# Optimization experiments

Measured on AMD Instinct MI355X. Metric: run time of the kernel, lower is better.

## Reference

```python
import jax, jax.numpy as jnp
import numpy as np

P, G, UV = 5, 40000, 256          # n_parts, gs_num (visible UV texels), uv_size
ZD, FD, HD = 32, 64, 32           # latent_z_dim, latent_f_dim, latent_h_dim
H1, L1 = 128, 3                   # mlp1 hidden dim, fc layers
H2, L2 = 128, 3                   # mlp2 hidden dim, fc layers
CC, LC = 64, 4                    # cnn hidden channels, cnn hidden layers


def _mlp_params(key, din, hid, nlayers, dout, nparts):
    ks = jax.random.split(key, 3)
    s = lambda f: 1.0 / np.sqrt(f)
    return dict(
        w_in=jax.random.normal(ks[0], (nparts, din, hid), jnp.float32) * s(din),
        b_in=jnp.zeros((nparts, hid), jnp.float32),
        w_hid=jax.random.normal(ks[1], (nparts, nlayers - 1, hid, hid), jnp.float32) * s(hid),
        b_hid=jnp.zeros((nparts, nlayers - 1, hid), jnp.float32),
        w_out=jax.random.normal(ks[2], (nparts, hid, dout), jnp.float32) * s(hid),
        b_out=jnp.zeros((nparts, dout), jnp.float32),
    )


def setup_inputs() -> dict:
    key = jax.random.key(0)
    ks = jax.random.split(key, 12)
    d1 = FD + ZD
    d2 = d1 + 3 + 11
    inp = {
        'latent_z': jax.random.normal(ks[2], (G, ZD), jnp.float32),
        'latent_f': jax.random.normal(ks[3], (P, FD), jnp.float32),
        'cano_xyz': jax.random.normal(ks[4], (G, 3), jnp.float32),
    }
    for k, v in _mlp_params(ks[0], d1, H1, L1, 11, P).items():
        inp['mlp1_' + k] = v
    for k, v in _mlp_params(ks[1], d2, H2, L2, HD, P).items():
        inp['mlp2_' + k] = v
    inp['conv_in_w'] = jax.random.normal(ks[5], (CC, HD, 3, 3), jnp.float32) * (1.0 / np.sqrt(HD * 9))
    inp['conv_in_b'] = jnp.zeros((CC,), jnp.float32)
    inp['conv_hid_w'] = jax.random.normal(ks[6], (LC - 1, CC, CC, 3, 3), jnp.float32) * (1.0 / np.sqrt(CC * 9))
    inp['conv_hid_b'] = jnp.zeros((LC - 1, CC), jnp.float32)
    inp['conv_out_w'] = jax.random.normal(ks[7], (3, CC, 3, 3), jnp.float32) * (1.0 / np.sqrt(CC * 9))
    inp['conv_out_b'] = jnp.zeros((3,), jnp.float32)
    inp['gs_part'] = jax.random.randint(ks[8], (G,), 0, P, jnp.int32)
    inp['uv_idx'] = jax.random.permutation(ks[9], UV * UV)[:G].astype(jnp.int32)  # unique visible texels
    return inp


def _part_mlp(x, w_in, b_in, w_hid, b_hid, w_out, b_out, part):
    # x: [G, D]; weights stacked over parts. Run every part's MLP, gather by part id.
    h = jax.nn.leaky_relu(jnp.einsum('gd,pdh->pgh', x, w_in) + b_in[:, None, :])
    for l in range(w_hid.shape[1]):
        h = jax.nn.leaky_relu(jnp.einsum('pgh,pho->pgo', h, w_hid[:, l]) + b_hid[:, l][:, None, :])
    out = jnp.einsum('pgh,pho->pgo', h, w_out) + b_out[:, None, :]  # [P, G, O]
    return out[part, jnp.arange(out.shape[1])]                       # [G, O]


def _conv(x, w, b):
    y = jax.lax.conv_general_dilated(x, w, (1, 1), 'SAME',
                                     dimension_numbers=('NCHW', 'OIHW', 'NCHW'))
    return y + b[None, :, None, None]


def _instance_norm(x, eps=1e-5):
    m = x.mean(axis=(2, 3), keepdims=True)
    v = x.var(axis=(2, 3), keepdims=True)
    return (x - m) / jnp.sqrt(v + eps)


def reference(latent_z, latent_f, cano_xyz,
              mlp1_w_in, mlp1_b_in, mlp1_w_hid, mlp1_b_hid, mlp1_w_out, mlp1_b_out,
              mlp2_w_in, mlp2_b_in, mlp2_w_hid, mlp2_b_hid, mlp2_w_out, mlp2_b_out,
              conv_in_w, conv_in_b, conv_hid_w, conv_hid_b, conv_out_w, conv_out_b,
              gs_part, uv_idx):
    feat_f = latent_f[gs_part]                                  # [G, FD] per-part feature gather
    x1 = jnp.concatenate([feat_f, latent_z], axis=-1)           # [G, FD+ZD]
    attrs = _part_mlp(x1, mlp1_w_in, mlp1_b_in, mlp1_w_hid, mlp1_b_hid,
                      mlp1_w_out, mlp1_b_out, gs_part)          # [G, 11] gaussian attrs
    x2 = jnp.concatenate([x1, cano_xyz, attrs], axis=-1)        # [G, FD+ZD+3+11]
    h = _part_mlp(x2, mlp2_w_in, mlp2_b_in, mlp2_w_hid, mlp2_b_hid,
                  mlp2_w_out, mlp2_b_out, gs_part)              # [G, HD]
    # scatter per-gaussian features back into the UV map (uvmask-indexed texels)
    uvmap = jnp.zeros((UV * UV, h.shape[-1]), h.dtype).at[uv_idx].add(h)
    x = uvmap.T.reshape(1, h.shape[-1], UV, UV)                 # [1, HD, UV, UV]
    # CNN refinement: conv -> (relu, conv, instance_norm) x (LC-1) -> conv -> sigmoid
    x = _conv(x, conv_in_w, conv_in_b)
    for l in range(conv_hid_w.shape[0]):
        x = _instance_norm(_conv(jax.nn.relu(x), conv_hid_w[l], conv_hid_b[l]))
    x = _conv(x, conv_out_w, conv_out_b)
    return jax.nn.sigmoid(x)                                    # [1, 3, UV, UV]
```

## Files before the change

### kernel.cpp

```cpp
#include <hip/hip_runtime.h>

#define G_N 40000
#define P_N 5
#define PIX 65536
#define XP 136
#define CIP 72

typedef short short8 __attribute__((ext_vector_type(8)));
typedef short short4v __attribute__((ext_vector_type(4)));
typedef float f32x4 __attribute__((ext_vector_type(4)));
#define MFMA16(a, b, c) __builtin_amdgcn_mfma_f32_16x16x32_bf16(a, b, c, 0, 0, 0)

__device__ __forceinline__ short f2b(float f) {
    unsigned u = __builtin_bit_cast(unsigned, f);
    unsigned r = (u + 0x7fffu + ((u >> 16) & 1u)) >> 16;
    return (short)r;
}
__device__ __forceinline__ float b2f(short s) {
    unsigned u = ((unsigned)(unsigned short)s) << 16;
    return __builtin_bit_cast(float, u);
}


__global__ __launch_bounds__(256) void hist_k(const int* __restrict__ part,
                                              int* __restrict__ counts, int n) {
    __shared__ int s_c[P_N];
    if (threadIdx.x < P_N) s_c[threadIdx.x] = 0;
    __syncthreads();
    int g = blockIdx.x * 256 + threadIdx.x;
    if (g < n) atomicAdd(&s_c[part[g]], 1);
    __syncthreads();
    if (threadIdx.x < P_N) atomicAdd(&counts[threadIdx.x], s_c[threadIdx.x]);
}

__global__ void offs_k(const int* __restrict__ counts, int* __restrict__ offs) {
    if (threadIdx.x == 0) {
        int o = 0;
        for (int p = 0; p < P_N; ++p) {
            offs[p] = o;
            o += (counts[p] + 127) & ~127;
        }
        offs[P_N] = o;
    }
}

__global__ __launch_bounds__(256) void scatter_k(const int* __restrict__ part,
                                                 const int* __restrict__ offs,
                                                 int* __restrict__ cursors,
                                                 int* __restrict__ perm, int n) {
    const int t = threadIdx.x;
    const int g = blockIdx.x * 256 + t;
    const int p = (g < n) ? part[g] : -1;
    const int lane = t & 63;
    const int wid = t >> 6;
    __shared__ int s_wc[4][P_N];
    __shared__ int s_base[P_N];
    const unsigned long long lmask = (1ull << lane) - 1ull;
    int myrank = 0;
    for (int pp = 0; pp < P_N; ++pp) {
        unsigned long long m = __ballot(p == pp);
        if (p == pp) myrank = __popcll(m & lmask);
        if (lane == 0) s_wc[wid][pp] = __popcll(m);
    }
    __syncthreads();
    if (t < P_N) {
        int tot = s_wc[0][t] + s_wc[1][t] + s_wc[2][t] + s_wc[3][t];
        s_base[t] = atomicAdd(&cursors[t], tot);
    }
    __syncthreads();
    if (g < n) {
        int pre = 0;
        #pragma unroll
        for (int w2 = 0; w2 < 4; ++w2) if (w2 < wid) pre += s_wc[w2][p];
        perm[offs[p] + s_base[p] + pre + myrank] = g;
    }
}


__device__ __forceinline__ float mseg(int l, const float* __restrict__ src,
                                      int DIN, int DOUT, int NP, int pps) {
    const int pn = NP * 128;
    const int p = l / pn;
    const int r = l - p * pn;
    const int n = r >> 7, k = r & 127;
    return (n < DOUT && k < DIN) ? src[p * pps + k * DOUT + n] : 0.f;
}
__device__ __forceinline__ float cseg(int l, const float* __restrict__ src, int CIN) {
    const int per = 9 * 64 * CIN;
    const int ll = l / per;
    int rem = l - ll * per;
    const int tap = rem / (64 * CIN);
    rem -= tap * 64 * CIN;
    const int och = rem / CIN;
    const int ci = rem - och * CIN;
    return src[((ll * 64 + och) * CIN + ci) * 9 + tap];
}

__global__ __launch_bounds__(256) void prep_k(
        const float* __restrict__ m1wi, const float* __restrict__ m1wh,
        const float* __restrict__ m1wo, const float* __restrict__ m2wi,
        const float* __restrict__ m2wh, const float* __restrict__ m2wo,
        const float* __restrict__ cinw, const float* __restrict__ chw,
        short* __restrict__ wb) {
    const int idx = blockIdx.x * 256 + threadIdx.x;
    if (idx >= 651264) return;
    float v;
    if      (idx < 81920)  v = mseg(idx,          m1wi,         96, 128, 128, 12288);
    else if (idx < 163840) v = mseg(idx - 81920,  m1wh,        128, 128, 128, 32768);
    else if (idx < 245760) v = mseg(idx - 163840, m1wh + 16384,128, 128, 128, 32768);
    else if (idx < 256000) v = mseg(idx - 245760, m1wo,        128,  11,  16, 1408);
    else if (idx < 337920) v = mseg(idx - 256000, m2wi,        110, 128, 128, 14080);
    else if (idx < 419840) v = mseg(idx - 337920, m2wh,        128, 128, 128, 32768);
    else if (idx < 501760) v = mseg(idx - 419840, m2wh + 16384,128, 128, 128, 32768);
    else if (idx < 522240) v = mseg(idx - 501760, m2wo,        128,  32,  32, 4096);
    else if (idx < 540672) v = cseg(idx - 522240, cinw, 32);
    else                   v = cseg(idx - 540672, chw, 64);
    wb[idx] = f2b(v);
}


template<int NKC, bool ACT>
__device__ __forceinline__ void dlayerSep(const short* __restrict__ wt,
                                          const float* __restrict__ bias,
                                          const short* src, short* dst, int m0, int n0) {
    const int lane = threadIdx.x & 63;
    const int ln = lane & 15, lq = lane >> 4;
    short8 B[4][NKC];
    float bs[4];
    #pragma unroll
    for (int nt = 0; nt < 4; ++nt) {
        #pragma unroll
        for (int kc = 0; kc < NKC; ++kc)
            B[nt][kc] = *(const short8*)(wt + (n0 + nt * 16 + ln) * 128 + kc * 32 + lq * 8);
        bs[nt] = bias[n0 + nt * 16 + ln];
    }
    #pragma unroll
    for (int mt = 0; mt < 4; ++mt) {
        short8 A[NKC];
        #pragma unroll
        for (int kc = 0; kc < NKC; ++kc)
            A[kc] = *(const short8*)(src + (m0 + mt * 16 + ln) * XP + kc * 32 + lq * 8);
        #pragma unroll
        for (int nt = 0; nt < 4; ++nt) {
            f32x4 acc = {bs[nt], bs[nt], bs[nt], bs[nt]};
            #pragma unroll
            for (int kc = 0; kc < NKC; ++kc)
                acc = MFMA16(A[kc], B[nt][kc], acc);
            #pragma unroll
            for (int r = 0; r < 4; ++r) {
                float v = acc[r];
                if (ACT) v = fmaxf(v, 0.01f * v);
                dst[(m0 + mt * 16 + lq * 4 + r) * XP + n0 + nt * 16 + ln] = f2b(v);
            }
        }
    }
}

template<bool ACT>
__device__ __forceinline__ void dlayerIP(const short* __restrict__ wt,
                                         const float* __restrict__ bias,
                                         short* buf, int m0, int n0) {
    const int lane = threadIdx.x & 63;
    const int ln = lane & 15, lq = lane >> 4;
    short8 A[4][4];
    #pragma unroll
    for (int mt = 0; mt < 4; ++mt)
        #pragma unroll
        for (int kc = 0; kc < 4; ++kc)
            A[mt][kc] = *(const short8*)(buf + (m0 + mt * 16 + ln) * XP + kc * 32 + lq * 8);
    __syncthreads();
    #pragma unroll
    for (int nt = 0; nt < 4; ++nt) {
        short8 B[4];
        #pragma unroll
        for (int kc = 0; kc < 4; ++kc)
            B[kc] = *(const short8*)(wt + (n0 + nt * 16 + ln) * 128 + kc * 32 + lq * 8);
        const float bs = bias[n0 + nt * 16 + ln];
        #pragma unroll
        for (int mt = 0; mt < 4; ++mt) {
            f32x4 acc = {bs, bs, bs, bs};
            #pragma unroll
            for (int kc = 0; kc < 4; ++kc)
                acc = MFMA16(A[mt][kc], B[kc], acc);
            #pragma unroll
            for (int r = 0; r < 4; ++r) {
                float v = acc[r];
                if (ACT) v = fmaxf(v, 0.01f * v);
                buf[(m0 + mt * 16 + lq * 4 + r) * XP + n0 + nt * 16 + ln] = f2b(v);
            }
        }
    }
    __syncthreads();
}

__global__ __launch_bounds__(256) void mlp_k(
        const float* __restrict__ latent_z, const float* __restrict__ latent_f,
        const float* __restrict__ cano,
        const short* __restrict__ wt1i, const float* __restrict__ b1i,
        const short* __restrict__ wt1h0, const short* __restrict__ wt1h1,
        const float* __restrict__ b1h,
        const short* __restrict__ wt1o, const float* __restrict__ b1o,
        const short* __restrict__ wt2i, const float* __restrict__ b2i,
        const short* __restrict__ wt2h0, const short* __restrict__ wt2h1,
        const float* __restrict__ b2h,
        const short* __restrict__ wt2o, const float* __restrict__ b2o,
        const int* __restrict__ uv_idx, const int* __restrict__ perm,
        const int* __restrict__ offs, const int* __restrict__ counts,
        unsigned short* __restrict__ uvmap ) {
    __shared__ short s_x[128 * XP];
    __shared__ short s_h[128 * XP];
    __shared__ int s_g[128];
    __shared__ int s_uv[128];

    const int t = threadIdx.x;
    const int lane = t & 63;
    const int w = t >> 6;
    const int ln = lane & 15, lq = lane >> 4;
    const int pos0 = blockIdx.x * 128;
    if (pos0 >= offs[P_N]) return;
    int p = 0;
    #pragma unroll
    for (int q = 1; q < P_N; ++q) if (pos0 >= offs[q]) p = q;
    const int vend = offs[p] + counts[p];

    if (t < 128) {
        const int pos = pos0 + t;
        const int g = (pos < vend) ? perm[pos] : -1;
        s_g[t] = g;
        s_uv[t] = (g >= 0) ? uv_idx[g] : 0;
    }
    __syncthreads();

    for (int i = t; i < 128 * 16; i += 256) {
        const int g = i >> 4, k4 = (i & 15) * 4;
        const float4 v = *(const float4*)(latent_f + p * 64 + k4);
        short4v o = {f2b(v.x), f2b(v.y), f2b(v.z), f2b(v.w)};
        *(short4v*)(s_x + g * XP + k4) = o;
    }
    for (int i = t; i < 128 * 8; i += 256) {
        const int g = i >> 3, k4 = (i & 7) * 4;
        const int gg = s_g[g];
        short4v o = {0, 0, 0, 0};
        if (gg >= 0) {
            const float4 v = *(const float4*)(latent_z + gg * 32 + k4);
            o[0] = f2b(v.x); o[1] = f2b(v.y); o[2] = f2b(v.z); o[3] = f2b(v.w);
        }
        *(short4v*)(s_x + g * XP + 64 + k4) = o;
    }
    for (int i = t; i < 128 * 3; i += 256) {
        const int g = i / 3, k = i - g * 3;
        const int gg = s_g[g];
        s_x[g * XP + 96 + k] = (gg >= 0) ? f2b(cano[gg * 3 + k]) : 0;
    }
    for (int i = t; i < 128 * 37; i += 256) {
        const int g = i / 37, k = 99 + (i - g * 37);
        s_x[g * XP + k] = 0;
    }
    __syncthreads();

    const int m0 = (w >> 1) * 64, n0 = (w & 1) * 64;

    dlayerSep<3, true>(wt1i + p * 16384, b1i + p * 128, s_x, s_h, m0, n0);
    __syncthreads();
    dlayerIP<true>(wt1h0 + p * 16384, b1h + (p * 2 + 0) * 128, s_h, m0, n0);
    dlayerIP<true>(wt1h1 + p * 16384, b1h + (p * 2 + 1) * 128, s_h, m0, n0);
    if ((w & 1) == 0) {
        short8 B[4];
        #pragma unroll
        for (int kc = 0; kc < 4; ++kc)
            B[kc] = *(const short8*)(wt1o + p * 2048 + ln * 128 + kc * 32 + lq * 8);
        const float bs = (ln < 11) ? b1o[p * 11 + ln] : 0.f;
        #pragma unroll
        for (int mt = 0; mt < 4; ++mt) {
            short8 A[4];
            #pragma unroll
            for (int kc = 0; kc < 4; ++kc)
                A[kc] = *(const short8*)(s_h + (m0 + mt * 16 + ln) * XP + kc * 32 + lq * 8);
            f32x4 acc = {bs, bs, bs, bs};
            #pragma unroll
            for (int kc = 0; kc < 4; ++kc) acc = MFMA16(A[kc], B[kc], acc);
            if (ln < 11) {
                #pragma unroll
                for (int r = 0; r < 4; ++r)
                    s_x[(m0 + mt * 16 + lq * 4 + r) * XP + 99 + ln] = f2b(acc[r]);
            }
        }
    }
    __syncthreads();

    dlayerSep<4, true>(wt2i + p * 16384, b2i + p * 128, s_x, s_h, m0, n0);
    __syncthreads();
    dlayerIP<true>(wt2h0 + p * 16384, b2h + (p * 2 + 0) * 128, s_h, m0, n0);
    dlayerIP<true>(wt2h1 + p * 16384, b2h + (p * 2 + 1) * 128, s_h, m0, n0);
    {
        const int nt0 = (w & 1) * 16;
        short8 B[4];
        #pragma unroll
        for (int kc = 0; kc < 4; ++kc)
            B[kc] = *(const short8*)(wt2o + p * 4096 + (nt0 + ln) * 128 + kc * 32 + lq * 8);
        const float bs = b2o[p * 32 + nt0 + ln];
        #pragma unroll
        for (int mt = 0; mt < 4; ++mt) {
            short8 A[4];
            #pragma unroll
            for (int kc = 0; kc < 4; ++kc)
                A[kc] = *(const short8*)(s_h + (m0 + mt * 16 + ln) * XP + kc * 32 + lq * 8);
            f32x4 acc = {bs, bs, bs, bs};
            #pragma unroll
            for (int kc = 0; kc < 4; ++kc) acc = MFMA16(A[kc], B[kc], acc);
            #pragma unroll
            for (int r = 0; r < 4; ++r) {
                const int m = m0 + mt * 16 + lq * 4 + r;
                const int g = s_g[m];
                if (g >= 0)
                    uvmap[s_uv[m] * 32 + nt0 + ln] = (unsigned short)f2b(acc[r]);
            }
        }
    }
}


template<int CIN, int TRANS, bool STATS>
__global__ __launch_bounds__(256) void conv_k(
        const unsigned short* __restrict__ in,
        const short* __restrict__ wt,
        const float* __restrict__ bias,
        const float* __restrict__ psum, const float* __restrict__ psq,
        unsigned short* __restrict__ out,
        float* __restrict__ ssum, float* __restrict__ ssq) {
    __shared__ short s_in[18 * 18 * CIP];
    __shared__ short s_w[2][64 * CIP];
    __shared__ float s_mr[2][64];

    const int t = threadIdx.x;
    const int lane = t & 63;
    const int w4 = t >> 6;
    const int ln = lane & 15, lq = lane >> 4;
    const int tx0 = blockIdx.x * 16, ty0 = blockIdx.y * 16;

    if (TRANS == 2 && t < 64) {
        const float m = psum[t] * (1.f / PIX);
        const float vv = psq[t] * (1.f / PIX) - m * m;
        s_mr[0][t] = m;
        s_mr[1][t] = rsqrtf(vv + 1e-5f);
    }
    __syncthreads();

    constexpr int RUNS = CIN / 8;
    for (int i = t; i < 324 * RUNS; i += 256) {
        const int sp = i / RUNS, run = i - sp * RUNS;
        const int r = sp / 18, c = sp - r * 18;
        const int gy = ty0 + r - 1, gx = tx0 + c - 1;
        short* dst = &s_in[(r * 18 + c) * CIP + run * 8];
        if (gy >= 0 && gy < 256 && gx >= 0 && gx < 256) {
            short8 v = *(const short8*)(in + ((gy * 256 + gx) * CIN + run * 8));
            if (TRANS == 0) {
                *(short8*)dst = v;
            } else {
                short8 o;
                #pragma unroll
                for (int j = 0; j < 8; ++j) {
                    float f = b2f(v[j]);
                    if (TRANS == 2) f = (f - s_mr[0][run * 8 + j]) * s_mr[1][run * 8 + j];
                    o[j] = f2b(fmaxf(f, 0.f));
                }
                *(short8*)dst = o;
            }
        } else {
            short8 z = {0, 0, 0, 0, 0, 0, 0, 0};
            *(short8*)dst = z;
        }
    }

    #define STAGEW(tap, buf)                                                     \
        for (int i = t; i < 64 * RUNS; i += 256) {                               \
            const int och = i / RUNS, run = i - och * RUNS;                      \
            *(short8*)&s_w[buf][och * CIP + run * 8] =                           \
                *(const short8*)(wt + ((tap) * 64 + och) * CIN + run * 8);       \
        }
    STAGEW(0, 0)
    __syncthreads();

    f32x4 acc[4][4];
    {
        float bs[4];
        #pragma unroll
        for (int nt = 0; nt < 4; ++nt) bs[nt] = bias[nt * 16 + ln];
        #pragma unroll
        for (int mt = 0; mt < 4; ++mt)
            #pragma unroll
            for (int nt = 0; nt < 4; ++nt) {
                f32x4 a = {bs[nt], bs[nt], bs[nt], bs[nt]};
                acc[mt][nt] = a;
            }
    }

    const int myrow = w4 * 4;
    for (int tap = 0; tap < 9; ++tap) {
        const int buf = tap & 1;
        if (tap + 1 < 9) { STAGEW(tap + 1, buf ^ 1) }
        const int dy = tap / 3, dx = tap % 3;
        #pragma unroll
        for (int kc = 0; kc < CIN / 32; ++kc) {
            short8 A[4], B[4];
            #pragma unroll
            for (int mt = 0; mt < 4; ++mt) {
                const int ry = myrow + mt + dy;
                const int rx = ln + dx;
                A[mt] = *(const short8*)&s_in[(ry * 18 + rx) * CIP + kc * 32 + lq * 8];
            }
            #pragma unroll
            for (int nt = 0; nt < 4; ++nt)
                B[nt] = *(const short8*)&s_w[buf][(nt * 16 + ln) * CIP + kc * 32 + lq * 8];
            #pragma unroll
            for (int mt = 0; mt < 4; ++mt)
                #pragma unroll
                for (int nt = 0; nt < 4; ++nt)
                    acc[mt][nt] = MFMA16(A[mt], B[nt], acc[mt][nt]);
        }
        __syncthreads();
    }
    #undef STAGEW

    #pragma unroll
    for (int nt = 0; nt < 4; ++nt) {
        float lsum = 0.f, lsqs = 0.f;
        #pragma unroll
        for (int mt = 0; mt < 4; ++mt) {
            const int gy = ty0 + myrow + mt;
            #pragma unroll
            for (int r = 0; r < 4; ++r) {
                const float v = acc[mt][nt][r];
                const int gx = tx0 + lq * 4 + r;
                out[(gy * 256 + gx) * 64 + nt * 16 + ln] = (unsigned short)f2b(v);
                if (STATS) { lsum += v; lsqs = fmaf(v, v, lsqs); }
            }
        }
        if (STATS) {
            lsum += __shfl_xor(lsum, 16, 64);
            lsum += __shfl_xor(lsum, 32, 64);
            lsqs += __shfl_xor(lsqs, 16, 64);
            lsqs += __shfl_xor(lsqs, 32, 64);
            if (lq == 0) {
                atomicAdd(&ssum[nt * 16 + ln], lsum);
                atomicAdd(&ssq[nt * 16 + ln], lsqs);
            }
        }
    }
}

__global__ __launch_bounds__(256) void convout_k(
        const unsigned short* __restrict__ in,
        const float* __restrict__ w,
        const float* __restrict__ bias,
        const float* __restrict__ psum, const float* __restrict__ psq,
        float* __restrict__ out) {
    __shared__ short s_in[18 * 18 * CIP];
    __shared__ float s_w[3][9][64];
    __shared__ float s_mr[2][64];

    const int t = threadIdx.x;
    const int tx0 = blockIdx.x * 16, ty0 = blockIdx.y * 16;
    if (t < 64) {
        const float m = psum[t] * (1.f / PIX);
        const float vv = psq[t] * (1.f / PIX) - m * m;
        s_mr[0][t] = m;
        s_mr[1][t] = rsqrtf(vv + 1e-5f);
    }
    __syncthreads();

    for (int i = t; i < 324 * 8; i += 256) {
        const int sp = i >> 3, run = i & 7;
        const int r = sp / 18, c = sp - r * 18;
        const int gy = ty0 + r - 1, gx = tx0 + c - 1;
        short* dst = &s_in[(r * 18 + c) * CIP + run * 8];
        if (gy >= 0 && gy < 256 && gx >= 0 && gx < 256) {
            short8 v = *(const short8*)(in + ((gy * 256 + gx) * 64 + run * 8));
            short8 o;
            #pragma unroll
            for (int j = 0; j < 8; ++j) {
                const float f = (b2f(v[j]) - s_mr[0][run * 8 + j]) * s_mr[1][run * 8 + j];
                o[j] = f2b(f);
            }
            *(short8*)dst = o;
        } else {
            short8 z = {0, 0, 0, 0, 0, 0, 0, 0};
            *(short8*)dst = z;
        }
    }
    for (int i = t; i < 1728; i += 256) {
        const int o = i / 576;
        const int rem = i - o * 576;
        const int tap = rem >> 6;
        const int ci = rem & 63;
        s_w[o][tap][ci] = w[o * 576 + ci * 9 + tap];
    }
    __syncthreads();

    const int py = t >> 4, px = t & 15;
    float a0 = bias[0], a1 = bias[1], a2 = bias[2];
    for (int tap = 0; tap < 9; ++tap) {
        const int dy = tap / 3, dx = tap % 3;
        const short* rp = &s_in[((py + dy) * 18 + (px + dx)) * CIP];
        #pragma unroll
        for (int c8 = 0; c8 < 8; ++c8) {
            short8 v = *(const short8*)(rp + c8 * 8);
            #pragma unroll
            for (int j = 0; j < 8; ++j) {
                const float f = b2f(v[j]);
                const int ci = c8 * 8 + j;
                a0 = fmaf(f, s_w[0][tap][ci], a0);
                a1 = fmaf(f, s_w[1][tap][ci], a1);
                a2 = fmaf(f, s_w[2][tap][ci], a2);
            }
        }
    }
    const int pix = (ty0 + py) * 256 + tx0 + px;
    out[pix]           = 1.f / (1.f + expf(-a0));
    out[PIX + pix]     = 1.f / (1.f + expf(-a1));
    out[2 * PIX + pix] = 1.f / (1.f + expf(-a2));
}


extern "C" void kernel_launch(void* const* d_in, const int* in_sizes, int n_in,
                              void* d_out, int out_size, void* d_ws, size_t ws_size,
                              hipStream_t stream) {
    (void)in_sizes; (void)n_in; (void)out_size; (void)ws_size;
    const float* latent_z = (const float*)d_in[0];
    const float* latent_f = (const float*)d_in[1];
    const float* cano     = (const float*)d_in[2];
    const float* m1wi = (const float*)d_in[3];
    const float* m1bi = (const float*)d_in[4];
    const float* m1wh = (const float*)d_in[5];
    const float* m1bh = (const float*)d_in[6];
    const float* m1wo = (const float*)d_in[7];
    const float* m1bo = (const float*)d_in[8];
    const float* m2wi = (const float*)d_in[9];
    const float* m2bi = (const float*)d_in[10];
    const float* m2wh = (const float*)d_in[11];
    const float* m2bh = (const float*)d_in[12];
    const float* m2wo = (const float*)d_in[13];
    const float* m2bo = (const float*)d_in[14];
    const float* cinw = (const float*)d_in[15];
    const float* cinb = (const float*)d_in[16];
    const float* chw  = (const float*)d_in[17];
    const float* chb  = (const float*)d_in[18];
    const float* cow  = (const float*)d_in[19];
    const float* cob  = (const float*)d_in[20];
    const int* gs_part = (const int*)d_in[21];
    const int* uv_idx  = (const int*)d_in[22];

    float* ws = (float*)d_ws;
    unsigned short* actA = (unsigned short*)ws;
    unsigned short* actB = (unsigned short*)(ws + 2097152);
    unsigned short* uvmap = actB;

    short* wb = (short*)(ws + 4194304);
    short* wt1i  = wb;
    short* wt1h0 = wb + 81920;
    short* wt1h1 = wb + 163840;
    short* wt1o  = wb + 245760;
    short* wt2i  = wb + 256000;
    short* wt2h0 = wb + 337920;
    short* wt2h1 = wb + 419840;
    short* wt2o  = wb + 501760;
    short* cwt_in  = wb + 522240;
    short* cwt_hid = wb + 540672;

    float* small = ws + 4194304 + 330000;
    int* counts  = (int*)small;
    int* cursors = counts + 8;
    int* offs    = cursors + 8;
    float* ssum  = small + 32;
    float* ssq   = ssum + 192;
    int* perm    = (int*)(ssq + 192);

    hipMemsetAsync(uvmap, 0, (size_t)PIX * 32 * sizeof(unsigned short), stream);
    hipMemsetAsync(small, 0, 1024 * sizeof(float), stream);

    hist_k<<<157, 256, 0, stream>>>(gs_part, counts, G_N);
    offs_k<<<1, 64, 0, stream>>>(counts, offs);
    scatter_k<<<157, 256, 0, stream>>>(gs_part, offs, cursors, perm, G_N);

    prep_k<<<2544, 256, 0, stream>>>(m1wi, m1wh, m1wo, m2wi, m2wh, m2wo, cinw, chw, wb);

    mlp_k<<<318, 256, 0, stream>>>(latent_z, latent_f, cano,
        wt1i, m1bi, wt1h0, wt1h1, m1bh, wt1o, m1bo,
        wt2i, m2bi, wt2h0, wt2h1, m2bh, wt2o, m2bo,
        uv_idx, perm, offs, counts, uvmap);

    dim3 cgrid(16, 16);
    conv_k<32, 0, false><<<cgrid, 256, 0, stream>>>(uvmap, cwt_in, cinb,
        nullptr, nullptr, actA, nullptr, nullptr);
    conv_k<64, 1, true><<<cgrid, 256, 0, stream>>>(actA, cwt_hid, chb,
        nullptr, nullptr, actB, ssum, ssq);
    conv_k<64, 2, true><<<cgrid, 256, 0, stream>>>(actB, cwt_hid + 36864, chb + 64,
        ssum, ssq, actA, ssum + 64, ssq + 64);
    conv_k<64, 2, true><<<cgrid, 256, 0, stream>>>(actA, cwt_hid + 73728, chb + 128,
        ssum + 64, ssq + 64, actB, ssum + 128, ssq + 128);
    convout_k<<<cgrid, 256, 0, stream>>>(actB, cow, cob,
        ssum + 128, ssq + 128, (float*)d_out);
}
```

Measured before the change: 304.1 us.

## Load conv weights directly from global into registers and double threads per tile

The 3x3 conv kernel no longer stages per-tap weights through double-buffered shared memory. Each wave now reads its B fragments straight from global memory (cache-resident) into registers, which removes the per-tap __syncthreads. Blocks grow to 512 threads, with each wave computing 2 rows instead of 4, and the input tile padding is sized to CIN. The intent is more waves per tile, fewer barriers and less LDS traffic, at the cost of repeated global or L2 weight loads and fewer accumulators per wave.

```diff
diff --git a/kernel.cpp b/kernel.cpp
--- a/kernel.cpp
+++ b/kernel.cpp
@@ -4,7 +4,6 @@
 #define P_N 5
 #define PIX 65536
 #define XP 136
-#define CIP 72
 
 typedef short short8 __attribute__((ext_vector_type(8)));
 typedef short short4v __attribute__((ext_vector_type(4)));
@@ -321,20 +320,19 @@
 
 
 template<int CIN, int TRANS, bool STATS>
-__global__ __launch_bounds__(256) void conv_k(
+__global__ __launch_bounds__(512) void conv_k(
         const unsigned short* __restrict__ in,
         const short* __restrict__ wt,
         const float* __restrict__ bias,
         const float* __restrict__ psum, const float* __restrict__ psq,
         unsigned short* __restrict__ out,
         float* __restrict__ ssum, float* __restrict__ ssq) {
-    __shared__ short s_in[18 * 18 * CIP];
-    __shared__ short s_w[2][64 * CIP];
+    constexpr int CS = CIN + 8;
+    __shared__ short s_in[18 * 18 * CS];
     __shared__ float s_mr[2][64];
 
     const int t = threadIdx.x;
     const int lane = t & 63;
-    const int w4 = t >> 6;
     const int ln = lane & 15, lq = lane >> 4;
     const int tx0 = blockIdx.x * 16, ty0 = blockIdx.y * 16;
 
@@ -344,14 +342,14 @@
         s_mr[0][t] = m;
         s_mr[1][t] = rsqrtf(vv + 1e-5f);
     }
-    __syncthreads();
+    if (TRANS == 2) __syncthreads();
 
     constexpr int RUNS = CIN / 8;
-    for (int i = t; i < 324 * RUNS; i += 256) {
+    for (int i = t; i < 324 * RUNS; i += 512) {
         const int sp = i / RUNS, run = i - sp * RUNS;
         const int r = sp / 18, c = sp - r * 18;
         const int gy = ty0 + r - 1, gx = tx0 + c - 1;
-        short* dst = &s_in[(r * 18 + c) * CIP + run * 8];
+        short* dst = &s_in[(r * 18 + c) * CS + run * 8];
         if (gy >= 0 && gy < 256 && gx >= 0 && gx < 256) {
             short8 v = *(const short8*)(in + ((gy * 256 + gx) * CIN + run * 8));
             if (TRANS == 0) {
@@ -371,23 +369,15 @@
             *(short8*)dst = z;
         }
     }
-
-    #define STAGEW(tap, buf)                                                     \
-        for (int i = t; i < 64 * RUNS; i += 256) {                               \
-            const int och = i / RUNS, run = i - och * RUNS;                      \
-            *(short8*)&s_w[buf][och * CIP + run * 8] =                           \
-                *(const short8*)(wt + ((tap) * 64 + och) * CIN + run * 8);       \
-        }
-    STAGEW(0, 0)
-    __syncthreads();
-
-    f32x4 acc[4][4];
+    __syncthreads();
+
+    f32x4 acc[2][4];
     {
         float bs[4];
         #pragma unroll
         for (int nt = 0; nt < 4; ++nt) bs[nt] = bias[nt * 16 + ln];
         #pragma unroll
-        for (int mt = 0; mt < 4; ++mt)
+        for (int mt = 0; mt < 2; ++mt)
             #pragma unroll
             for (int nt = 0; nt < 4; ++nt) {
                 f32x4 a = {bs[nt], bs[nt], bs[nt], bs[nt]};
@@ -395,39 +385,37 @@
             }
     }
 
-    const int myrow = w4 * 4;
+    const int r0 = (t >> 6) * 2;
+    #pragma unroll 3
     for (int tap = 0; tap < 9; ++tap) {
-        const int buf = tap & 1;
-        if (tap + 1 < 9) { STAGEW(tap + 1, buf ^ 1) }
         const int dy = tap / 3, dx = tap % 3;
+        const short* wtap = wt + tap * 64 * CIN;
+        short8 B[CIN / 32][4];
+        #pragma unroll
+        for (int kc = 0; kc < CIN / 32; ++kc)
+            #pragma unroll
+            for (int nt = 0; nt < 4; ++nt)
+                B[kc][nt] = *(const short8*)(wtap + (nt * 16 + ln) * CIN + kc * 32 + lq * 8);
         #pragma unroll
         for (int kc = 0; kc < CIN / 32; ++kc) {
-            short8 A[4], B[4];
-            #pragma unroll
-            for (int mt = 0; mt < 4; ++mt) {
-                const int ry = myrow + mt + dy;
-                const int rx = ln + dx;
-                A[mt] = *(const short8*)&s_in[(ry * 18 + rx) * CIP + kc * 32 + lq * 8];
-            }
-            #pragma unroll
-            for (int nt = 0; nt < 4; ++nt)
-                B[nt] = *(const short8*)&s_w[buf][(nt * 16 + ln) * CIP + kc * 32 + lq * 8];
-            #pragma unroll
-            for (int mt = 0; mt < 4; ++mt)
+            short8 A[2];
+            #pragma unroll
+            for (int mt = 0; mt < 2; ++mt)
+                A[mt] = *(const short8*)&s_in[((r0 + mt + dy) * 18 + ln + dx) * CS + kc * 32 + lq * 8];
+            #pragma unroll
+            for (int mt = 0; mt < 2; ++mt)
                 #pragma unroll
                 for (int nt = 0; nt < 4; ++nt)
-                    acc[mt][nt] = MFMA16(A[mt], B[nt], acc[mt][nt]);
-        }
-        __syncthreads();
-    }
-    #undef STAGEW
+                    acc[mt][nt] = MFMA16(A[mt], B[kc][nt], acc[mt][nt]);
+        }
+    }
 
     #pragma unroll
     for (int nt = 0; nt < 4; ++nt) {
         float lsum = 0.f, lsqs = 0.f;
         #pragma unroll
-        for (int mt = 0; mt < 4; ++mt) {
-            const int gy = ty0 + myrow + mt;
+        for (int mt = 0; mt < 2; ++mt) {
+            const int gy = ty0 + r0 + mt;
             #pragma unroll
             for (int r = 0; r < 4; ++r) {
                 const float v = acc[mt][nt][r];
@@ -455,7 +443,8 @@
         const float* __restrict__ bias,
         const float* __restrict__ psum, const float* __restrict__ psq,
         float* __restrict__ out) {
-    __shared__ short s_in[18 * 18 * CIP];
+    constexpr int CS = 72;
+    __shared__ short s_in[18 * 18 * CS];
     __shared__ float s_w[3][9][64];
     __shared__ float s_mr[2][64];
 
@@ -473,7 +462,7 @@
         const int sp = i >> 3, run = i & 7;
         const int r = sp / 18, c = sp - r * 18;
         const int gy = ty0 + r - 1, gx = tx0 + c - 1;
-        short* dst = &s_in[(r * 18 + c) * CIP + run * 8];
+        short* dst = &s_in[(r * 18 + c) * CS + run * 8];
         if (gy >= 0 && gy < 256 && gx >= 0 && gx < 256) {
             short8 v = *(const short8*)(in + ((gy * 256 + gx) * 64 + run * 8));
             short8 o;
@@ -501,7 +490,7 @@
     float a0 = bias[0], a1 = bias[1], a2 = bias[2];
     for (int tap = 0; tap < 9; ++tap) {
         const int dy = tap / 3, dx = tap % 3;
-        const short* rp = &s_in[((py + dy) * 18 + (px + dx)) * CIP];
+        const short* rp = &s_in[((py + dy) * 18 + (px + dx)) * CS];
         #pragma unroll
         for (int c8 = 0; c8 < 8; ++c8) {
             short8 v = *(const short8*)(rp + c8 * 8);
@@ -590,13 +579,13 @@
         uv_idx, perm, offs, counts, uvmap);
 
     dim3 cgrid(16, 16);
-    conv_k<32, 0, false><<<cgrid, 256, 0, stream>>>(uvmap, cwt_in, cinb,
+    conv_k<32, 0, false><<<cgrid, 512, 0, stream>>>(uvmap, cwt_in, cinb,
         nullptr, nullptr, actA, nullptr, nullptr);
-    conv_k<64, 1, true><<<cgrid, 256, 0, stream>>>(actA, cwt_hid, chb,
+    conv_k<64, 1, true><<<cgrid, 512, 0, stream>>>(actA, cwt_hid, chb,
         nullptr, nullptr, actB, ssum, ssq);
-    conv_k<64, 2, true><<<cgrid, 256, 0, stream>>>(actB, cwt_hid + 36864, chb + 64,
+    conv_k<64, 2, true><<<cgrid, 512, 0, stream>>>(actB, cwt_hid + 36864, chb + 64,
         ssum, ssq, actA, ssum + 64, ssq + 64);
-    conv_k<64, 2, true><<<cgrid, 256, 0, stream>>>(actA, cwt_hid + 73728, chb + 128,
+    conv_k<64, 2, true><<<cgrid, 512, 0, stream>>>(actA, cwt_hid + 73728, chb + 128,
         ssum + 64, ssq + 64, actB, ssum + 128, ssq + 128);
     convout_k<<<cgrid, 256, 0, stream>>>(actB, cow, cob,
         ssum + 128, ssq + 128, (float*)d_out);
```

Result: slower. 380.6 us (+25.1%).
